# Optimization experiments

Measured on AMD Instinct MI355X. Metric: run time of the kernel, lower is better.

The kernel has to match this reference:

```python
import jax, jax.numpy as jnp
import numpy as np

N_HEADS = 8
TANH_CLIPPING = 10.0
TEMP = 1.0


def setup_inputs() -> dict:
    key = jax.random.key(0)
    ks = jax.random.split(key, 8)
    B, N, D, CTX = 256, 1000, 128, 130
    embeddings = jax.random.normal(ks[0], (B, N, D), dtype=jnp.float32)
    step_context = jax.random.normal(ks[1], (B, 1, CTX), dtype=jnp.float32)
    mask = jax.random.randint(ks[2], (B, 1, N), 0, 2).astype(bool)
    # ensure at least one feasible node per row (node 0 always feasible)
    mask = mask.at[:, :, 0].set(False)
    W_node = jax.random.normal(ks[3], (D, 3 * D), dtype=jnp.float32) * (1.0 / np.sqrt(D))
    W_fixed = jax.random.normal(ks[4], (D, D), dtype=jnp.float32) * (1.0 / np.sqrt(D))
    W_step = jax.random.normal(ks[5], (CTX, D), dtype=jnp.float32) * (1.0 / np.sqrt(CTX))
    W_out = jax.random.normal(ks[6], (D, D), dtype=jnp.float32) * (1.0 / np.sqrt(D))
    return {"embeddings": embeddings, "step_context": step_context, "mask": mask,
            "W_node": W_node, "W_fixed": W_fixed, "W_step": W_step, "W_out": W_out}


def reference(embeddings, step_context, mask, W_node, W_fixed, W_step, W_out):
    # embeddings: [B, N, D], step_context: [B, 1, D+2], mask: [B, 1, N] (True = infeasible)
    B, N, D = embeddings.shape
    H = N_HEADS
    hd = D // H
    # _precompute: fixed context from graph mean, and K/V/logit_key from node embeddings
    graph_embed = embeddings.mean(axis=1)                       # [B, D]
    fixed_context = graph_embed @ W_fixed                       # [B, D]
    kvl = embeddings @ W_node                                   # [B, N, 3D]
    glimpse_k, glimpse_v, logit_k = jnp.split(kvl, 3, axis=-1)  # each [B, N, D]
    # query = fixed context + projected step context             [B, 1, D]
    query = fixed_context[:, None, :] + step_context @ W_step
    # multi-head glimpse attention (q_len = 1)
    q = query.reshape(B, 1, H, hd).transpose(0, 2, 1, 3)        # [B, H, 1, hd]
    K = glimpse_k.reshape(B, N, H, hd).transpose(0, 2, 1, 3)    # [B, H, N, hd]
    V = glimpse_v.reshape(B, N, H, hd).transpose(0, 2, 1, 3)    # [B, H, N, hd]
    compat = jnp.einsum('bhqd,bhnd->bhqn', q, K) / jnp.sqrt(jnp.float32(hd))
    # mask_inner
    compat = jnp.where(mask[:, None, :, :], -jnp.inf, compat)
    attn = jax.nn.softmax(compat, axis=-1)                      # [B, H, 1, N]
    heads = jnp.einsum('bhqn,bhnd->bhqd', attn, V)              # [B, H, 1, hd]
    glimpse = heads.transpose(0, 2, 1, 3).reshape(B, 1, D) @ W_out  # [B, 1, D]
    # single-head logits against logit_key, tanh-clipped
    logits = jnp.einsum('bqd,bnd->bqn', glimpse, logit_k) / jnp.sqrt(jnp.float32(D))
    logits = jnp.tanh(logits) * TANH_CLIPPING
    # mask_logits
    logits = jnp.where(mask, -jnp.inf, logits)
    log_p = jax.nn.log_softmax(logits / TEMP, axis=-1)          # [B, 1, N]
    return log_p
```

## Files before the change

### kernel.cpp

```cpp
#include <hip/hip_runtime.h>
#include <math.h>

#define NN   1000
#define DD   128
#define CTXN 130
#define NEG_BIG (-1.0e30f)


__global__ __launch_bounds__(1024, 4)
void k1_fused(const float* __restrict__ emb, const float* __restrict__ stepc,
              const void* __restrict__ maskp,
              const float* __restrict__ Wn, const float* __restrict__ Wf,
              const float* __restrict__ Ws,
              float* __restrict__ qpt, int* __restrict__ idxv, int* __restrict__ cntv) {
    const int b = blockIdx.x, t = threadIdx.x;
    const int w = t >> 6, lane = t & 63;
    const float* eb = emb + (size_t)b * (NN * DD);
    __shared__ __align__(16) float S[4096];
    __shared__ float s_mean[128], s_q[128];
    __shared__ int s_misint;
    __shared__ unsigned long long s_bal[16];
    __shared__ int s_woff[16];
    if (t == 0) {
        const unsigned char* mb8 = (const unsigned char*)maskp;
        int any = 0;
        for (int k = 0; k < 64; ++k) any |= mb8[4 * k + 1];
        s_misint = (any == 0) ? 1 : 0;
    }
    {
        const int c4 = t & 31, g = t >> 5;
        float4 a = make_float4(0.f, 0.f, 0.f, 0.f);
        for (int r = g; r < NN; r += 32) {
            const float4 v = *(const float4*)(eb + (size_t)r * DD + c4 * 4);
            a.x += v.x; a.y += v.y; a.z += v.z; a.w += v.w;
        }
        ((float4*)S)[g * 32 + c4] = a;
    }
    __syncthreads();
    if (t < 128) {
        float v = 0.f;
        #pragma unroll
        for (int g = 0; g < 32; ++g) v += S[g * 128 + t];
        s_mean[t] = v * (1.0f / (float)NN);
    }
    __syncthreads();
    {
        const int d = t & 127, p = t >> 7;
        float a = 0.f;
        for (int i = 16 * p; i < 16 * p + 16; ++i)
            a = fmaf(s_mean[i], Wf[i * DD + d], a);
        const float* scb = stepc + (size_t)b * CTXN;
        const int c0 = 16 * p, c1 = (p == 7) ? CTXN : 16 * p + 16;
        for (int c = c0; c < c1; ++c)
            a = fmaf(scb[c], Ws[c * DD + d], a);
        S[p * 128 + d] = a;
    }
    __syncthreads();
    if (t < 128) {
        float v = 0.f;
        #pragma unroll
        for (int p = 0; p < 8; ++p) v += S[p * 128 + t];
        s_q[t] = v;
    }
    __syncthreads();
    {
        const int i = t & 127, h = t >> 7;
        float a = 0.f;
        #pragma unroll
        for (int j = 0; j < 16; ++j)
            a = fmaf(Wn[i * 384 + h * 16 + j], s_q[h * 16 + j], a);
        qpt[(size_t)b * 1024 + h * 128 + i] = a * 0.25f;
    }
    {
        const unsigned char* mk8 = (const unsigned char*)maskp + (size_t)b * NN;
        const int* mk32 = (const int*)maskp + (size_t)b * NN;
        int um = 0;
        if (t < NN) um = s_misint ? (mk32[t] == 0) : (mk8[t] == 0);
        const unsigned long long bal = __ballot(um);
        if (lane == 0) s_bal[w] = bal;
        __syncthreads();
        if (t == 0) {
            int o = 0;
            #pragma unroll
            for (int w2 = 0; w2 < 16; ++w2) {
                s_woff[w2] = o;
                o += (int)__popcll(s_bal[w2]);
            }
            cntv[b] = o;
        }
        __syncthreads();
        if (um) {
            const int pos = s_woff[w] +
                (int)__popcll(bal & ((lane == 0) ? 0ULL : (~0ULL >> (64 - lane))));
            idxv[(size_t)b * 1024 + pos] = t;
        }
    }
}

__global__ __launch_bounds__(512, 2)
void kB_stream(const float* __restrict__ emb, const float* __restrict__ qpt,
               const int* __restrict__ idxv, const int* __restrict__ cntv,
               float* __restrict__ wembp, float* __restrict__ stats) {
    const int b = blockIdx.x >> 3, s = blockIdx.x & 7;
    const int t = threadIdx.x, w = t >> 6, lane = t & 63;
    const int rg = lane >> 4, cl = lane & 15;
    const int row_sel = rg >> 1, hh = rg & 1;
    const int cnt = cntv[b];
    const int lo = (s * cnt) >> 3;
    const int hi = ((s + 1) * cnt) >> 3;
    const int nrows = hi - lo;
    const float* eb = emb + (size_t)b * (NN * DD);
    __shared__ __align__(16) float s_qpT[1024];
    __shared__ __align__(16) float s_part[8 * 8 * 132];
    __shared__ float s_sumw[64];
    __shared__ int s_idx[128];
    for (int i = t; i < 1024; i += 512) s_qpT[i] = qpt[(size_t)b * 1024 + i];
    if (t < 128) s_idx[t] = (t < nrows) ? idxv[(size_t)b * 1024 + lo + t] : 0;
    __syncthreads();
    float4 qa[4], qb[4];
    #pragma unroll
    for (int hp = 0; hp < 4; ++hp) {
        const int h = hh * 4 + hp;
        qa[hp] = *(const float4*)&s_qpT[h * 128 + cl * 8];
        qb[hp] = *(const float4*)&s_qpT[h * 128 + cl * 8 + 4];
    }
    float4 accA[4] = {}, accB[4] = {};
    float psum[4] = {0.f, 0.f, 0.f, 0.f};
    const int niter = (nrows + 15) >> 4;
    for (int it = 0; it < niter; ++it) {
        const int rp = it * 16 + w * 2 + row_sel;
        const bool valid = (rp < nrows);
        const int n = s_idx[rp & 127];
        float4 e0 = make_float4(0.f, 0.f, 0.f, 0.f), e1 = e0;
        if (valid) {
            e0 = *(const float4*)(eb + (size_t)n * DD + cl * 8);
            e1 = *(const float4*)(eb + (size_t)n * DD + cl * 8 + 4);
        }
        float cp[4];
        #pragma unroll
        for (int hp = 0; hp < 4; ++hp) {
            float a = e0.x * qa[hp].x;
            a = fmaf(e0.y, qa[hp].y, a);
            a = fmaf(e0.z, qa[hp].z, a);
            a = fmaf(e0.w, qa[hp].w, a);
            a = fmaf(e1.x, qb[hp].x, a);
            a = fmaf(e1.y, qb[hp].y, a);
            a = fmaf(e1.z, qb[hp].z, a);
            a = fmaf(e1.w, qb[hp].w, a);
            cp[hp] = a;
        }
        #pragma unroll
        for (int hp = 0; hp < 4; ++hp) {
            cp[hp] += __shfl_xor(cp[hp], 1, 16);
            cp[hp] += __shfl_xor(cp[hp], 2, 16);
            cp[hp] += __shfl_xor(cp[hp], 4, 16);
            cp[hp] += __shfl_xor(cp[hp], 8, 16);
        }
        #pragma unroll
        for (int hp = 0; hp < 4; ++hp) {
            const float p = valid ? expf(fminf(cp[hp], 80.f)) : 0.f;
            psum[hp] += p;
            accA[hp].x = fmaf(p, e0.x, accA[hp].x);
            accA[hp].y = fmaf(p, e0.y, accA[hp].y);
            accA[hp].z = fmaf(p, e0.z, accA[hp].z);
            accA[hp].w = fmaf(p, e0.w, accA[hp].w);
            accB[hp].x = fmaf(p, e1.x, accB[hp].x);
            accB[hp].y = fmaf(p, e1.y, accB[hp].y);
            accB[hp].z = fmaf(p, e1.z, accB[hp].z);
            accB[hp].w = fmaf(p, e1.w, accB[hp].w);
        }
    }
    #pragma unroll
    for (int hp = 0; hp < 4; ++hp) {
        accA[hp].x += __shfl_xor(accA[hp].x, 32, 64);
        accA[hp].y += __shfl_xor(accA[hp].y, 32, 64);
        accA[hp].z += __shfl_xor(accA[hp].z, 32, 64);
        accA[hp].w += __shfl_xor(accA[hp].w, 32, 64);
        accB[hp].x += __shfl_xor(accB[hp].x, 32, 64);
        accB[hp].y += __shfl_xor(accB[hp].y, 32, 64);
        accB[hp].z += __shfl_xor(accB[hp].z, 32, 64);
        accB[hp].w += __shfl_xor(accB[hp].w, 32, 64);
        psum[hp]   += __shfl_xor(psum[hp], 32, 64);
    }
    if (rg < 2) {
        #pragma unroll
        for (int hp = 0; hp < 4; ++hp) {
            const int h = rg * 4 + hp;
            *(float4*)&s_part[(w * 8 + h) * 132 + cl * 8]     = accA[hp];
            *(float4*)&s_part[(w * 8 + h) * 132 + cl * 8 + 4] = accB[hp];
            if (cl == 0) s_sumw[w * 8 + h] = psum[hp];
        }
    }
    __syncthreads();
    for (int i = t; i < 1024; i += 512) {
        const int h = i >> 7, c = i & 127;
        float v = 0.f;
        #pragma unroll
        for (int w2 = 0; w2 < 8; ++w2) v += s_part[(w2 * 8 + h) * 132 + c];
        wembp[(size_t)b * 8192 + s * 1024 + i] = v;
    }
    if (t < 8) {
        float v = 0.f;
        #pragma unroll
        for (int w2 = 0; w2 < 8; ++w2) v += s_sumw[w2 * 8 + t];
        stats[(size_t)b * 64 + s * 8 + t] = v;
    }
}

__global__ __launch_bounds__(1024, 4)
void k4_fused(const float* __restrict__ emb, const float* __restrict__ wembp,
              const float* __restrict__ stats,
              const float* __restrict__ Wn, const float* __restrict__ Wo,
              const int* __restrict__ idxv, const int* __restrict__ cntv,
              float* __restrict__ out) {
    const int b = blockIdx.x, t = threadIdx.x;
    const int w = t >> 6, lane = t & 63;
    const int rg = lane >> 4, cl = lane & 15;
    const float* eb = emb + (size_t)b * (NN * DD);
    __shared__ float s_dinv[8];
    __shared__ float s_wemb[8 * 130];
    __shared__ __align__(16) float s_red[1024];
    __shared__ float s_h[128], s_gl[128], s_g2[128];
    __shared__ float s_logits[1000];
    __shared__ int s_idxf[1024];
    __shared__ float s_r2[32];
    __shared__ float s_lse;
    const int cnt = cntv[b];
    if (t < NN) s_logits[t] = NEG_BIG;
    s_idxf[t] = (t < cnt) ? idxv[(size_t)b * 1024 + t] : 0;
    if (t < 8) {
        float den = 0.f;
        #pragma unroll
        for (int ss = 0; ss < 8; ++ss) den += stats[(size_t)b * 64 + ss * 8 + t];
        s_dinv[t] = 1.0f / den;
    }
    __syncthreads();
    {
        const int h = t >> 7, i = t & 127;
        float v = 0.f;
        #pragma unroll
        for (int ss = 0; ss < 8; ++ss)
            v += wembp[(size_t)b * 8192 + ss * 1024 + t];
        s_wemb[h * 130 + i] = v * s_dinv[h];
    }
    __syncthreads();
    {
        const int j = t & 127, p = t >> 7;
        float a = 0.f;
        for (int i = 16 * p; i < 16 * p + 16; ++i)
            a = fmaf(Wn[i * 384 + 128 + j], s_wemb[(j >> 4) * 130 + i], a);
        s_red[p * 128 + j] = a;
    }
    __syncthreads();
    if (t < 128) {
        float v = 0.f;
        #pragma unroll
        for (int p = 0; p < 8; ++p) v += s_red[p * 128 + t];
        s_h[t] = v;
    }
    __syncthreads();
    {
        const int d = t & 127, p = t >> 7;
        float a = 0.f;
        for (int j = 16 * p; j < 16 * p + 16; ++j)
            a = fmaf(s_h[j], Wo[j * DD + d], a);
        s_red[p * 128 + d] = a;
    }
    __syncthreads();
    if (t < 128) {
        float v = 0.f;
        #pragma unroll
        for (int p = 0; p < 8; ++p) v += s_red[p * 128 + t];
        s_gl[t] = v;
    }
    __syncthreads();
    {
        const int i = t & 127, p = t >> 7;
        float a = 0.f;
        for (int d = 16 * p; d < 16 * p + 16; ++d)
            a = fmaf(Wn[i * 384 + 256 + d], s_gl[d], a);
        s_red[p * 128 + i] = a;
    }
    __syncthreads();
    if (t < 128) {
        float v = 0.f;
        #pragma unroll
        for (int p = 0; p < 8; ++p) v += s_red[p * 128 + t];
        s_g2[t] = v * 0.08838834764831845f;
    }
    __syncthreads();
    {
        const float4 ga = *(const float4*)&s_g2[cl * 8];
        const float4 gb = *(const float4*)&s_g2[cl * 8 + 4];
        for (int it = 0; it < 16; ++it) {
            const int pos = it * 64 + w * 4 + rg;
            const bool valid = (pos < cnt);
            const int n = s_idxf[pos];
            float a = 0.f;
            if (valid) {
                const float4 e0 = *(const float4*)(eb + (size_t)n * DD + cl * 8);
                const float4 e1 = *(const float4*)(eb + (size_t)n * DD + cl * 8 + 4);
                a = e0.x * ga.x;
                a = fmaf(e0.y, ga.y, a);
                a = fmaf(e0.z, ga.z, a);
                a = fmaf(e0.w, ga.w, a);
                a = fmaf(e1.x, gb.x, a);
                a = fmaf(e1.y, gb.y, a);
                a = fmaf(e1.z, gb.z, a);
                a = fmaf(e1.w, gb.w, a);
            }
            a += __shfl_xor(a, 1, 16);
            a += __shfl_xor(a, 2, 16);
            a += __shfl_xor(a, 4, 16);
            a += __shfl_xor(a, 8, 16);
            if (cl == 0 && valid)
                s_logits[n] = 10.0f * tanhf(a);
        }
    }
    __syncthreads();
    {
        float m = NEG_BIG;
        if (t < NN) m = s_logits[t];
        #pragma unroll
        for (int o = 32; o; o >>= 1) m = fmaxf(m, __shfl_xor(m, o, 64));
        if (lane == 0) s_r2[w] = m;
        __syncthreads();
        if (t == 0) {
            float mm = s_r2[0];
            #pragma unroll
            for (int i = 1; i < 16; ++i) mm = fmaxf(mm, s_r2[i]);
            s_r2[16] = mm;
        }
        __syncthreads();
        const float mb = s_r2[16];
        float sum = (t < NN) ? expf(s_logits[t] - mb) : 0.f;
        #pragma unroll
        for (int o = 32; o; o >>= 1) sum += __shfl_xor(sum, o, 64);
        __syncthreads();
        if (lane == 0) s_r2[w] = sum;
        __syncthreads();
        if (t == 0) {
            float ss = 0.f;
            #pragma unroll
            for (int i = 0; i < 16; ++i) ss += s_r2[i];
            s_lse = mb + logf(ss);
        }
        __syncthreads();
        if (t < NN) out[(size_t)b * NN + t] = s_logits[t] - s_lse;
    }
}

extern "C" void kernel_launch(void* const* d_in, const int* in_sizes, int n_in,
                              void* d_out, int out_size, void* d_ws, size_t ws_size,
                              hipStream_t stream) {
    const float* emb   = (const float*)d_in[0];
    const float* stepc = (const float*)d_in[1];
    const void*  mask  = (const void*)d_in[2];
    const float* Wn = (const float*)d_in[3];
    const float* Wf = (const float*)d_in[4];
    const float* Ws = (const float*)d_in[5];
    const float* Wo = (const float*)d_in[6];
    float* out = (float*)d_out;
    const int B = in_sizes[0] / (NN * DD);

    float* wsf = (float*)d_ws;
    const size_t n_qpt   = (size_t)B * 1024;
    const size_t n_wembp = (size_t)B * 8192;
    const size_t n_stats = (size_t)B * 64;
    const size_t n_idx   = (size_t)B * 1024;

    float* qpt   = wsf;
    float* wembp = qpt + n_qpt;
    float* stats = wembp + n_wembp;
    int*   idxv  = (int*)(stats + n_stats);
    int*   cntv  = idxv + n_idx;

    k1_fused <<<B,     1024, 0, stream>>>(emb, stepc, mask, Wn, Wf, Ws, qpt, idxv, cntv);
    kB_stream<<<B * 8, 512,  0, stream>>>(emb, qpt, idxv, cntv, wembp, stats);
    k4_fused <<<B,     1024, 0, stream>>>(emb, wembp, stats, Wn, Wo, idxv, cntv, out);
}
```

Before: 93.24 us.

## Remap kB_stream lanes to one row per wave with two heads per lane

```diff
diff --git a/kernel.cpp b/kernel.cpp
--- a/kernel.cpp
+++ b/kernel.cpp
@@ -97,14 +97,13 @@
     }
 }
 
-__global__ __launch_bounds__(512, 2)
+__global__ __launch_bounds__(512, 4)
 void kB_stream(const float* __restrict__ emb, const float* __restrict__ qpt,
                const int* __restrict__ idxv, const int* __restrict__ cntv,
                float* __restrict__ wembp, float* __restrict__ stats) {
     const int b = blockIdx.x >> 3, s = blockIdx.x & 7;
     const int t = threadIdx.x, w = t >> 6, lane = t & 63;
     const int rg = lane >> 4, cl = lane & 15;
-    const int row_sel = rg >> 1, hh = rg & 1;
     const int cnt = cntv[b];
     const int lo = (s * cnt) >> 3;
     const int hi = ((s + 1) * cnt) >> 3;
@@ -117,80 +116,53 @@
     for (int i = t; i < 1024; i += 512) s_qpT[i] = qpt[(size_t)b * 1024 + i];
     if (t < 128) s_idx[t] = (t < nrows) ? idxv[(size_t)b * 1024 + lo + t] : 0;
     __syncthreads();
-    float4 qa[4], qb[4];
-    #pragma unroll
-    for (int hp = 0; hp < 4; ++hp) {
-        const int h = hh * 4 + hp;
-        qa[hp] = *(const float4*)&s_qpT[h * 128 + cl * 8];
-        qb[hp] = *(const float4*)&s_qpT[h * 128 + cl * 8 + 4];
-    }
-    float4 accA[4] = {}, accB[4] = {};
-    float psum[4] = {0.f, 0.f, 0.f, 0.f};
-    const int niter = (nrows + 15) >> 4;
+    const int h0 = 2 * rg, h1 = 2 * rg + 1;
+    const float4 qa0 = *(const float4*)&s_qpT[h0 * 128 + cl * 8];
+    const float4 qa1 = *(const float4*)&s_qpT[h0 * 128 + cl * 8 + 4];
+    const float4 qb0 = *(const float4*)&s_qpT[h1 * 128 + cl * 8];
+    const float4 qb1 = *(const float4*)&s_qpT[h1 * 128 + cl * 8 + 4];
+    float4 a0A = make_float4(0.f,0.f,0.f,0.f), a0B = a0A;
+    float4 a1A = a0A, a1B = a0A;
+    float ps0 = 0.f, ps1 = 0.f;
+    const int niter = (nrows + 7) >> 3;
     for (int it = 0; it < niter; ++it) {
-        const int rp = it * 16 + w * 2 + row_sel;
+        const int rp = it * 8 + w;
         const bool valid = (rp < nrows);
         const int n = s_idx[rp & 127];
-        float4 e0 = make_float4(0.f, 0.f, 0.f, 0.f), e1 = e0;
+        float4 e0 = make_float4(0.f,0.f,0.f,0.f), e1 = e0;
         if (valid) {
             e0 = *(const float4*)(eb + (size_t)n * DD + cl * 8);
             e1 = *(const float4*)(eb + (size_t)n * DD + cl * 8 + 4);
         }
-        float cp[4];
-        #pragma unroll
-        for (int hp = 0; hp < 4; ++hp) {
-            float a = e0.x * qa[hp].x;
-            a = fmaf(e0.y, qa[hp].y, a);
-            a = fmaf(e0.z, qa[hp].z, a);
-            a = fmaf(e0.w, qa[hp].w, a);
-            a = fmaf(e1.x, qb[hp].x, a);
-            a = fmaf(e1.y, qb[hp].y, a);
-            a = fmaf(e1.z, qb[hp].z, a);
-            a = fmaf(e1.w, qb[hp].w, a);
-            cp[hp] = a;
-        }
-        #pragma unroll
-        for (int hp = 0; hp < 4; ++hp) {
-            cp[hp] += __shfl_xor(cp[hp], 1, 16);
-            cp[hp] += __shfl_xor(cp[hp], 2, 16);
-            cp[hp] += __shfl_xor(cp[hp], 4, 16);
-            cp[hp] += __shfl_xor(cp[hp], 8, 16);
-        }
-        #pragma unroll
-        for (int hp = 0; hp < 4; ++hp) {
-            const float p = valid ? expf(fminf(cp[hp], 80.f)) : 0.f;
-            psum[hp] += p;
-            accA[hp].x = fmaf(p, e0.x, accA[hp].x);
-            accA[hp].y = fmaf(p, e0.y, accA[hp].y);
-            accA[hp].z = fmaf(p, e0.z, accA[hp].z);
-            accA[hp].w = fmaf(p, e0.w, accA[hp].w);
-            accB[hp].x = fmaf(p, e1.x, accB[hp].x);
-            accB[hp].y = fmaf(p, e1.y, accB[hp].y);
-            accB[hp].z = fmaf(p, e1.z, accB[hp].z);
-            accB[hp].w = fmaf(p, e1.w, accB[hp].w);
-        }
-    }
-    #pragma unroll
-    for (int hp = 0; hp < 4; ++hp) {
-        accA[hp].x += __shfl_xor(accA[hp].x, 32, 64);
-        accA[hp].y += __shfl_xor(accA[hp].y, 32, 64);
-        accA[hp].z += __shfl_xor(accA[hp].z, 32, 64);
-        accA[hp].w += __shfl_xor(accA[hp].w, 32, 64);
-        accB[hp].x += __shfl_xor(accB[hp].x, 32, 64);
-        accB[hp].y += __shfl_xor(accB[hp].y, 32, 64);
-        accB[hp].z += __shfl_xor(accB[hp].z, 32, 64);
-        accB[hp].w += __shfl_xor(accB[hp].w, 32, 64);
-        psum[hp]   += __shfl_xor(psum[hp], 32, 64);
-    }
-    if (rg < 2) {
-        #pragma unroll
-        for (int hp = 0; hp < 4; ++hp) {
-            const int h = rg * 4 + hp;
-            *(float4*)&s_part[(w * 8 + h) * 132 + cl * 8]     = accA[hp];
-            *(float4*)&s_part[(w * 8 + h) * 132 + cl * 8 + 4] = accB[hp];
-            if (cl == 0) s_sumw[w * 8 + h] = psum[hp];
-        }
-    }
+        float c0 = e0.x * qa0.x;
+        c0 = fmaf(e0.y, qa0.y, c0); c0 = fmaf(e0.z, qa0.z, c0); c0 = fmaf(e0.w, qa0.w, c0);
+        c0 = fmaf(e1.x, qa1.x, c0); c0 = fmaf(e1.y, qa1.y, c0);
+        c0 = fmaf(e1.z, qa1.z, c0); c0 = fmaf(e1.w, qa1.w, c0);
+        float c1 = e0.x * qb0.x;
+        c1 = fmaf(e0.y, qb0.y, c1); c1 = fmaf(e0.z, qb0.z, c1); c1 = fmaf(e0.w, qb0.w, c1);
+        c1 = fmaf(e1.x, qb1.x, c1); c1 = fmaf(e1.y, qb1.y, c1);
+        c1 = fmaf(e1.z, qb1.z, c1); c1 = fmaf(e1.w, qb1.w, c1);
+        c0 += __shfl_xor(c0, 1, 16); c1 += __shfl_xor(c1, 1, 16);
+        c0 += __shfl_xor(c0, 2, 16); c1 += __shfl_xor(c1, 2, 16);
+        c0 += __shfl_xor(c0, 4, 16); c1 += __shfl_xor(c1, 4, 16);
+        c0 += __shfl_xor(c0, 8, 16); c1 += __shfl_xor(c1, 8, 16);
+        const float p0 = valid ? expf(fminf(c0, 80.f)) : 0.f;
+        const float p1 = valid ? expf(fminf(c1, 80.f)) : 0.f;
+        ps0 += p0; ps1 += p1;
+        a0A.x = fmaf(p0, e0.x, a0A.x); a0A.y = fmaf(p0, e0.y, a0A.y);
+        a0A.z = fmaf(p0, e0.z, a0A.z); a0A.w = fmaf(p0, e0.w, a0A.w);
+        a0B.x = fmaf(p0, e1.x, a0B.x); a0B.y = fmaf(p0, e1.y, a0B.y);
+        a0B.z = fmaf(p0, e1.z, a0B.z); a0B.w = fmaf(p0, e1.w, a0B.w);
+        a1A.x = fmaf(p1, e0.x, a1A.x); a1A.y = fmaf(p1, e0.y, a1A.y);
+        a1A.z = fmaf(p1, e0.z, a1A.z); a1A.w = fmaf(p1, e0.w, a1A.w);
+        a1B.x = fmaf(p1, e1.x, a1B.x); a1B.y = fmaf(p1, e1.y, a1B.y);
+        a1B.z = fmaf(p1, e1.z, a1B.z); a1B.w = fmaf(p1, e1.w, a1B.w);
+    }
+    *(float4*)&s_part[(w * 8 + h0) * 132 + cl * 8]     = a0A;
+    *(float4*)&s_part[(w * 8 + h0) * 132 + cl * 8 + 4] = a0B;
+    *(float4*)&s_part[(w * 8 + h1) * 132 + cl * 8]     = a1A;
+    *(float4*)&s_part[(w * 8 + h1) * 132 + cl * 8 + 4] = a1B;
+    if (cl == 0) { s_sumw[w * 8 + h0] = ps0; s_sumw[w * 8 + h1] = ps1; }
     __syncthreads();
     for (int i = t; i < 1024; i += 512) {
         const int h = i >> 7, c = i & 127;
```

After: 82.99 us. 1.12x faster.
